# Optimization experiments

Measured on AMD Instinct MI355X. Metric: run time of the kernel, lower is better.

## Reference

```python
import jax, jax.numpy as jnp
import numpy as np

V, E, H = 32000, 256, 512
B, S, T = 32, 128, 64


def setup_inputs() -> dict:
    key = jax.random.key(0)
    ks = jax.random.split(key, 16)
    sc = 0.02
    n = lambda k, shp: (jax.random.normal(k, shp, jnp.float32) * sc)
    return {
        "src": jax.random.randint(ks[0], (B, S), 0, V),
        "tgt": jax.random.randint(ks[1], (B, T), 0, V),
        "embed": n(ks[2], (V, E)),
        "enc_Wih": n(ks[3], (4 * H, E)),
        "enc_Whh": n(ks[4], (4 * H, H)),
        "enc_bih": n(ks[5], (4 * H,)),
        "enc_bhh": n(ks[6], (4 * H,)),
        "dec_Wih": n(ks[7], (4 * H, E + H)),
        "dec_Whh": n(ks[8], (4 * H, H)),
        "dec_bih": n(ks[9], (4 * H,)),
        "dec_bhh": n(ks[10], (4 * H,)),
        "attn_W": n(ks[11], (H, 2 * H)),
        "attn_b": n(ks[12], (H,)),
        "attn_v": jax.random.uniform(ks[13], (H,), jnp.float32),  # torch.rand init
        "fc_W": n(ks[14], (V, H)),
        "fc_b": n(ks[15], (V,)),
    }


def lstm_step(x, h, c, Wih, Whh, bih, bhh):
    # PyTorch gate order: i, f, g, o
    gates = x @ Wih.T + h @ Whh.T + (bih + bhh)
    i, f, g, o = jnp.split(gates, 4, axis=-1)
    c = jax.nn.sigmoid(f) * c + jax.nn.sigmoid(i) * jnp.tanh(g)
    h = jax.nn.sigmoid(o) * jnp.tanh(c)
    return h, c


def reference(src, tgt, embed, enc_Wih, enc_Whh, enc_bih, enc_bhh,
              dec_Wih, dec_Whh, dec_bih, dec_bhh,
              attn_W, attn_b, attn_v, fc_W, fc_b):
    Bsz = src.shape[0]
    Hd = enc_Whh.shape[1]
    src_emb = embed[src]                      # [B,S,E]
    h0 = jnp.zeros((Bsz, Hd), jnp.float32)
    c0 = jnp.zeros((Bsz, Hd), jnp.float32)

    def enc_step(carry, x_t):
        h, c = carry
        h, c = lstm_step(x_t, h, c, enc_Wih, enc_Whh, enc_bih, enc_bhh)
        return (h, c), h

    (h, c), enc_hs = jax.lax.scan(enc_step, (h0, c0), src_emb.transpose(1, 0, 2))
    enc_out = enc_hs.transpose(1, 0, 2)       # [B,S,H]

    # split attn linear: W_attn @ cat(h, enc) = W_h @ h + W_e @ enc; precompute enc part
    W_h, W_e = attn_W[:, :Hd], attn_W[:, Hd:]
    enc_proj = jnp.einsum('bsh,kh->bsk', enc_out, W_e) + attn_b  # [B,S,H]

    dec_in = embed[tgt[:, :-1]]               # [B,T-1,E]

    def dec_step(carry, x_t):
        h, c = carry
        energy = jnp.tanh((h @ W_h.T)[:, None, :] + enc_proj)    # [B,S,H]
        scores = jnp.einsum('bsh,h->bs', energy, attn_v)
        w = jax.nn.softmax(scores, axis=1)
        context = jnp.einsum('bs,bsh->bh', w, enc_out)
        h, c = lstm_step(jnp.concatenate([x_t, context], axis=1), h, c,
                         dec_Wih, dec_Whh, dec_bih, dec_bhh)
        return (h, c), h

    (_, _), hs = jax.lax.scan(dec_step, (h, c), dec_in.transpose(1, 0, 2))
    outputs = jnp.einsum('tbh,vh->btv', hs, fc_W) + fc_b          # [B,T-1,V]
    return outputs
```

## Files before the change

### kernel.cpp

```cpp
#include <hip/hip_runtime.h>
#include <cstdint>
#include <cstddef>

typedef __bf16 bf16;
typedef __bf16 bf16x8 __attribute__((ext_vector_type(8)));
typedef __bf16 bf16x4 __attribute__((ext_vector_type(4)));
typedef float  f32x4  __attribute__((ext_vector_type(4)));

#define NV 32000
#define NE 256
#define NH 512
#define NB 32
#define NS 128
#define NT 64
#define NTD 63
#define G4H 2048

__device__ __forceinline__ float sigf(float x) {
    return 1.0f / (1.0f + __expf(-x));
}
__device__ __forceinline__ float tanhf_(float x) {
    return 1.0f - 2.0f / (__expf(2.0f * x) + 1.0f);
}

__global__ void k_cast_fcW(const float* __restrict__ src, bf16* __restrict__ dst, int n4) {
    int i = blockIdx.x * 256 + threadIdx.x;
    if (i < n4) {
        float4 v = *(const float4*)(src + 4 * (size_t)i);
        bf16x4 o;
        o[0] = (bf16)v.x; o[1] = (bf16)v.y; o[2] = (bf16)v.z; o[3] = (bf16)v.w;
        *(bf16x4*)(dst + 4 * (size_t)i) = o;
    }
}

__global__ void k_cast_small(const float* __restrict__ encWih, const float* __restrict__ decWih,
                             const float* __restrict__ attnW,
                             const float* __restrict__ ebih, const float* __restrict__ ebhh,
                             const float* __restrict__ dbih, const float* __restrict__ dbhh,
                             bf16* __restrict__ encWihB, bf16* __restrict__ decWihXB,
                             bf16* __restrict__ attnWeB,
                             float* __restrict__ bsumE, float* __restrict__ bsumD,
                             float* __restrict__ cbuf) {
    int i = blockIdx.x * 256 + threadIdx.x;
    const int n1 = G4H * NE;
    const int n2 = G4H * NE;
    const int n3 = NH * NH;
    if (i < n1) { encWihB[i] = (bf16)encWih[i]; return; }
    i -= n1;
    if (i < n2) { int r = i >> 8, c = i & 255; decWihXB[i] = (bf16)decWih[(size_t)r * 768 + c]; return; }
    i -= n2;
    if (i < n3) { int r = i >> 9, c = i & 511; attnWeB[i] = (bf16)attnW[(size_t)r * 1024 + 512 + c]; return; }
    i -= n3;
    if (i < G4H) { bsumE[i] = ebih[i] + ebhh[i]; return; }
    i -= G4H;
    if (i < G4H) { bsumD[i] = dbih[i] + dbhh[i]; return; }
    i -= G4H;
    if (i < NB * NH) { cbuf[i] = 0.0f; return; }
}

__global__ void k_embed(const int* __restrict__ src, const int* __restrict__ tgt,
                        const float* __restrict__ embed,
                        bf16* __restrict__ srcE, bf16* __restrict__ decE) {
    int i = blockIdx.x * 256 + threadIdx.x;
    const int nS = NB * NS * NE;
    if (i < nS) {
        int r = i >> 8, e = i & 255;
        srcE[i] = (bf16)embed[(size_t)src[r] * NE + e];
        return;
    }
    i -= nS;
    const int nD = NB * NTD * NE;
    if (i < nD) {
        int r = i >> 8, e = i & 255;
        int bb = r / NTD, tt = r % NTD;
        decE[i] = (bf16)embed[(size_t)tgt[bb * NT + tt] * NE + e];
    }
}

__global__ __launch_bounds__(256) void k_gemm(const bf16* __restrict__ A,
                                              const bf16* __restrict__ Bw,
                                              const float* __restrict__ bias,
                                              float* __restrict__ C,
                                              int M, int N, int K) {
    const int bn = blockIdx.x * 128;
    const int bm = blockIdx.y * 128;
    const int tid = threadIdx.x;
    __shared__ bf16 As[128 * 72];
    __shared__ bf16 Bs[128 * 72];
    const int wave = tid >> 6, lane = tid & 63;
    const int wm = (wave >> 1) * 64, wn = (wave & 1) * 64;
    const int r16 = lane & 15, quad = lane >> 4;

    f32x4 acc[4][4];
#pragma unroll
    for (int i = 0; i < 4; i++)
#pragma unroll
        for (int j = 0; j < 4; j++)
#pragma unroll
            for (int e = 0; e < 4; e++) acc[i][j][e] = 0.0f;

    for (int kb = 0; kb < K; kb += 64) {
#pragma unroll
        for (int i = 0; i < 4; i++) {
            int ci = tid + i * 256;
            int row = ci >> 3, kc = (ci & 7) * 8;
            bf16x8 va;
#pragma unroll
            for (int z = 0; z < 8; z++) va[z] = (bf16)0.0f;
            int gr = bm + row;
            if (gr < M) va = *(const bf16x8*)(A + (size_t)gr * K + kb + kc);
            *(bf16x8*)(As + row * 72 + kc) = va;
            bf16x8 vb = *(const bf16x8*)(Bw + (size_t)(bn + row) * K + kb + kc);
            *(bf16x8*)(Bs + row * 72 + kc) = vb;
        }
        __syncthreads();
#pragma unroll
        for (int ks = 0; ks < 2; ks++) {
            bf16x8 af[4], bfr[4];
#pragma unroll
            for (int mi = 0; mi < 4; mi++)
                af[mi] = *(const bf16x8*)(As + (wm + mi * 16 + r16) * 72 + ks * 32 + quad * 8);
#pragma unroll
            for (int ni = 0; ni < 4; ni++)
                bfr[ni] = *(const bf16x8*)(Bs + (wn + ni * 16 + r16) * 72 + ks * 32 + quad * 8);
#pragma unroll
            for (int mi = 0; mi < 4; mi++)
#pragma unroll
                for (int ni = 0; ni < 4; ni++)
                    acc[mi][ni] = __builtin_amdgcn_mfma_f32_16x16x32_bf16(af[mi], bfr[ni], acc[mi][ni], 0, 0, 0);
        }
        __syncthreads();
    }
#pragma unroll
    for (int mi = 0; mi < 4; mi++) {
#pragma unroll
        for (int e = 0; e < 4; e++) {
            int row = bm + wm + mi * 16 + quad * 4 + e;
            if (row < M) {
#pragma unroll
                for (int ni = 0; ni < 4; ni++) {
                    int col = bn + wn + ni * 16 + r16;
                    C[(size_t)row * N + col] = acc[mi][ni][e] + bias[col];
                }
            }
        }
    }
}

__global__ __launch_bounds__(256) void k_enc_step(const float* __restrict__ Xenc,
                                                  const float* __restrict__ Whh,
                                                  float* __restrict__ enc_out,
                                                  bf16* __restrict__ enc_out_b,
                                                  float* __restrict__ cbuf, int t) {
    const int blk = blockIdx.x;
    const int d0 = blk * 4;
    const int tid = threadIdx.x;
    __shared__ float wl[16 * 516];
    __shared__ float gl[16 * 33];

#pragma unroll
    for (int i = 0; i < 8; i++) {
        int ci = tid + i * 256;
        int ri = ci >> 7, kc = (ci & 127) * 4;
        int j = ((ri >> 2) * NH) + d0 + (ri & 3);
        *(float4*)(wl + ri * 516 + kc) = *(const float4*)(Whh + (size_t)j * NH + kc);
    }
    __syncthreads();

    const int b = tid >> 3, rl = tid & 7;
    float a0 = 0.0f, a1 = 0.0f;
    if (t > 0) {
        const float* hb = enc_out + ((size_t)(b * NS + t - 1)) * NH;
        const float* w0 = wl + rl * 516;
        const float* w1 = wl + (rl + 8) * 516;
        for (int kc = 0; kc < NH; kc += 4) {
            float4 h4 = *(const float4*)(hb + kc);
            float4 x0 = *(const float4*)(w0 + kc);
            float4 x1 = *(const float4*)(w1 + kc);
            a0 += h4.x * x0.x + h4.y * x0.y + h4.z * x0.z + h4.w * x0.w;
            a1 += h4.x * x1.x + h4.y * x1.y + h4.z * x1.z + h4.w * x1.w;
        }
    }
    {
        int j0 = ((rl >> 2) * NH) + d0 + (rl & 3);
        int j1 = (((rl + 8) >> 2) * NH) + d0 + ((rl + 8) & 3);
        const float* xr = Xenc + ((size_t)(b * NS + t)) * G4H;
        a0 += xr[j0];
        a1 += xr[j1];
        gl[rl * 33 + b] = a0;
        gl[(rl + 8) * 33 + b] = a1;
    }
    __syncthreads();
    if (tid < 128) {
        int bb = tid & 31, dl = tid >> 5;
        float gi = gl[(0 * 4 + dl) * 33 + bb];
        float gf = gl[(1 * 4 + dl) * 33 + bb];
        float gg = gl[(2 * 4 + dl) * 33 + bb];
        float go = gl[(3 * 4 + dl) * 33 + bb];
        int d = d0 + dl;
        float c_old = cbuf[bb * NH + d];
        float cn = sigf(gf) * c_old + sigf(gi) * tanhf_(gg);
        float hn = sigf(go) * tanhf_(cn);
        cbuf[bb * NH + d] = cn;
        size_t oi = ((size_t)(bb * NS + t)) * NH + d;
        enc_out[oi] = hn;
        enc_out_b[oi] = (bf16)hn;
    }
}

__global__ __launch_bounds__(256) void k_dec_mm1(const float* __restrict__ decWhh,
                                                 const float* __restrict__ attnW,
                                                 const float* __restrict__ enc_out,
                                                 const float* __restrict__ hbuf,
                                                 float* __restrict__ Gp,
                                                 float* __restrict__ hWh, int t) {
    const int blk = blockIdx.x;
    const int tid = threadIdx.x;
    __shared__ float wl[16 * 516];
    const bool gatePart = blk < 128;

#pragma unroll
    for (int i = 0; i < 8; i++) {
        int ci = tid + i * 256;
        int ri = ci >> 7, kc = (ci & 127) * 4;
        const float* srcp;
        if (gatePart) srcp = decWhh + (size_t)(blk * 16 + ri) * NH + kc;
        else          srcp = attnW + (size_t)((blk - 128) * 16 + ri) * 1024 + kc;
        *(float4*)(wl + ri * 516 + kc) = *(const float4*)srcp;
    }
    __syncthreads();

    const int b = tid >> 3, rl = tid & 7;
    const float* hb;
    if (t == 0) hb = enc_out + ((size_t)(b * NS + NS - 1)) * NH;
    else        hb = hbuf + (size_t)b * NH;
    const float* w0 = wl + rl * 516;
    const float* w1 = wl + (rl + 8) * 516;
    float a0 = 0.0f, a1 = 0.0f;
    for (int kc = 0; kc < NH; kc += 4) {
        float4 h4 = *(const float4*)(hb + kc);
        float4 x0 = *(const float4*)(w0 + kc);
        float4 x1 = *(const float4*)(w1 + kc);
        a0 += h4.x * x0.x + h4.y * x0.y + h4.z * x0.z + h4.w * x0.w;
        a1 += h4.x * x1.x + h4.y * x1.y + h4.z * x1.z + h4.w * x1.w;
    }
    if (gatePart) {
        int j0 = blk * 16 + rl;
        Gp[b * G4H + j0] = a0;
        Gp[b * G4H + j0 + 8] = a1;
    } else {
        int r0 = (blk - 128) * 16 + rl;
        hWh[b * NH + r0] = a0;
        hWh[b * NH + r0 + 8] = a1;
    }
}

__global__ __launch_bounds__(256) void k_dec_attn(const float* __restrict__ hWh,
                                                  const float* __restrict__ attn_v,
                                                  const float* __restrict__ enc_proj,
                                                  const float* __restrict__ enc_out,
                                                  float* __restrict__ ctx) {
    const int b = blockIdx.x;
    const int tid = threadIdx.x;
    __shared__ float hw[512], vv[512], ps[256], sc[128], red[64];
    hw[tid] = hWh[b * NH + tid];
    hw[tid + 256] = hWh[b * NH + tid + 256];
    vv[tid] = attn_v[tid];
    vv[tid + 256] = attn_v[tid + 256];
    __syncthreads();

    const int s = tid >> 1, hf = tid & 1;
    const float* ep = enc_proj + ((size_t)(b * NS + s)) * NH + hf * 256;
    const float* hwp = hw + hf * 256;
    const float* vvp = vv + hf * 256;
    float p = 0.0f;
    for (int k = 0; k < 256; k += 4) {
        float4 e = *(const float4*)(ep + k);
        p += tanhf_(hwp[k + 0] + e.x) * vvp[k + 0];
        p += tanhf_(hwp[k + 1] + e.y) * vvp[k + 1];
        p += tanhf_(hwp[k + 2] + e.z) * vvp[k + 2];
        p += tanhf_(hwp[k + 3] + e.w) * vvp[k + 3];
    }
    ps[tid] = p;
    __syncthreads();
    if (tid < 128) sc[tid] = ps[2 * tid] + ps[2 * tid + 1];
    __syncthreads();
    if (tid < 64) red[tid] = fmaxf(sc[tid], sc[tid + 64]);
    __syncthreads();
    if (tid < 32) red[tid] = fmaxf(red[tid], red[tid + 32]);
    __syncthreads();
    if (tid < 16) red[tid] = fmaxf(red[tid], red[tid + 16]);
    __syncthreads();
    if (tid < 8) red[tid] = fmaxf(red[tid], red[tid + 8]);
    __syncthreads();
    if (tid < 4) red[tid] = fmaxf(red[tid], red[tid + 4]);
    __syncthreads();
    if (tid < 2) red[tid] = fmaxf(red[tid], red[tid + 2]);
    __syncthreads();
    if (tid == 0) red[0] = fmaxf(red[0], red[1]);
    __syncthreads();
    float mx = red[0];
    __syncthreads();
    if (tid < 128) sc[tid] = __expf(sc[tid] - mx);
    __syncthreads();
    if (tid < 64) red[tid] = sc[tid] + sc[tid + 64];
    __syncthreads();
    if (tid < 32) red[tid] = red[tid] + red[tid + 32];
    __syncthreads();
    if (tid < 16) red[tid] = red[tid] + red[tid + 16];
    __syncthreads();
    if (tid < 8) red[tid] = red[tid] + red[tid + 8];
    __syncthreads();
    if (tid < 4) red[tid] = red[tid] + red[tid + 4];
    __syncthreads();
    if (tid < 2) red[tid] = red[tid] + red[tid + 2];
    __syncthreads();
    if (tid == 0) red[0] = red[0] + red[1];
    __syncthreads();
    float inv = 1.0f / red[0];
    __syncthreads();
    if (tid < 128) sc[tid] *= inv;
    __syncthreads();
#pragma unroll
    for (int half = 0; half < 2; half++) {
        int k = tid + half * 256;
        float a = 0.0f;
        const float* eo = enc_out + ((size_t)(b * NS)) * NH + k;
        for (int s2 = 0; s2 < NS; s2++) a += sc[s2] * eo[(size_t)s2 * NH];
        ctx[b * NH + k] = a;
    }
}

__global__ __launch_bounds__(256) void k_dec_final(const float* __restrict__ Xdec,
                                                   const float* __restrict__ decWih,
                                                   const float* __restrict__ Gp,
                                                   const float* __restrict__ ctx,
                                                   float* __restrict__ cbuf,
                                                   float* __restrict__ hbuf,
                                                   bf16* __restrict__ hs_b, int t) {
    const int blk = blockIdx.x;
    const int d0 = blk * 4;
    const int tid = threadIdx.x;
    __shared__ float wl[16 * 516];
    __shared__ float gl[16 * 33];

#pragma unroll
    for (int i = 0; i < 8; i++) {
        int ci = tid + i * 256;
        int ri = ci >> 7, kc = (ci & 127) * 4;
        int j = ((ri >> 2) * NH) + d0 + (ri & 3);
        *(float4*)(wl + ri * 516 + kc) = *(const float4*)(decWih + (size_t)j * 768 + 256 + kc);
    }
    __syncthreads();

    const int b = tid >> 3, rl = tid & 7;
    const float* cb = ctx + (size_t)b * NH;
    const float* w0 = wl + rl * 516;
    const float* w1 = wl + (rl + 8) * 516;
    float a0 = 0.0f, a1 = 0.0f;
    for (int kc = 0; kc < NH; kc += 4) {
        float4 h4 = *(const float4*)(cb + kc);
        float4 x0 = *(const float4*)(w0 + kc);
        float4 x1 = *(const float4*)(w1 + kc);
        a0 += h4.x * x0.x + h4.y * x0.y + h4.z * x0.z + h4.w * x0.w;
        a1 += h4.x * x1.x + h4.y * x1.y + h4.z * x1.z + h4.w * x1.w;
    }
    {
        int j0 = ((rl >> 2) * NH) + d0 + (rl & 3);
        int j1 = (((rl + 8) >> 2) * NH) + d0 + ((rl + 8) & 3);
        const float* xr = Xdec + ((size_t)(b * NTD + t)) * G4H;
        a0 += xr[j0] + Gp[b * G4H + j0];
        a1 += xr[j1] + Gp[b * G4H + j1];
        gl[rl * 33 + b] = a0;
        gl[(rl + 8) * 33 + b] = a1;
    }
    __syncthreads();
    if (tid < 128) {
        int bb = tid & 31, dl = tid >> 5;
        float gi = gl[(0 * 4 + dl) * 33 + bb];
        float gf = gl[(1 * 4 + dl) * 33 + bb];
        float gg = gl[(2 * 4 + dl) * 33 + bb];
        float go = gl[(3 * 4 + dl) * 33 + bb];
        int d = d0 + dl;
        float c_old = cbuf[bb * NH + d];
        float cn = sigf(gf) * c_old + sigf(gi) * tanhf_(gg);
        float hn = sigf(go) * tanhf_(cn);
        cbuf[bb * NH + d] = cn;
        hbuf[bb * NH + d] = hn;
        hs_b[((size_t)(bb * NTD + t)) * NH + d] = (bf16)hn;
    }
}

extern "C" void kernel_launch(void* const* d_in, const int* in_sizes, int n_in,
                              void* d_out, int out_size, void* d_ws, size_t ws_size,
                              hipStream_t stream) {
    const int* src = (const int*)d_in[0];
    const int* tgt = (const int*)d_in[1];
    const float* embed = (const float*)d_in[2];
    const float* encWih = (const float*)d_in[3];
    const float* encWhh = (const float*)d_in[4];
    const float* encbih = (const float*)d_in[5];
    const float* encbhh = (const float*)d_in[6];
    const float* decWih = (const float*)d_in[7];
    const float* decWhh = (const float*)d_in[8];
    const float* decbih = (const float*)d_in[9];
    const float* decbhh = (const float*)d_in[10];
    const float* attnW = (const float*)d_in[11];
    const float* attnb = (const float*)d_in[12];
    const float* attnv = (const float*)d_in[13];
    const float* fcW = (const float*)d_in[14];
    const float* fcb = (const float*)d_in[15];
    float* out = (float*)d_out;

    char* w = (char*)d_ws;
    auto alloc = [&](size_t bytes) -> char* {
        char* p = w;
        w += (bytes + 255) & ~(size_t)255;
        return p;
    };
    bf16* fcWB     = (bf16*)alloc((size_t)NV * NH * 2);
    bf16* encWihB  = (bf16*)alloc((size_t)G4H * NE * 2);
    bf16* decWihXB = (bf16*)alloc((size_t)G4H * NE * 2);
    bf16* attnWeB  = (bf16*)alloc((size_t)NH * NH * 2);
    bf16* srcE     = (bf16*)alloc((size_t)NB * NS * NE * 2);
    bf16* decE     = (bf16*)alloc((size_t)NB * NTD * NE * 2);
    float* bsumE   = (float*)alloc((size_t)G4H * 4);
    float* bsumD   = (float*)alloc((size_t)G4H * 4);
    float* Xenc    = (float*)alloc((size_t)NB * NS * G4H * 4);
    float* Xdec    = (float*)alloc((size_t)NB * NTD * G4H * 4);
    float* enc_out = (float*)alloc((size_t)NB * NS * NH * 4);
    bf16* enc_outB = (bf16*)alloc((size_t)NB * NS * NH * 2);
    float* encproj = (float*)alloc((size_t)NB * NS * NH * 4);
    float* cbuf    = (float*)alloc((size_t)NB * NH * 4);
    float* hbuf    = (float*)alloc((size_t)NB * NH * 4);
    float* Gp      = (float*)alloc((size_t)NB * G4H * 4);
    float* hWh     = (float*)alloc((size_t)NB * NH * 4);
    float* ctx     = (float*)alloc((size_t)NB * NH * 4);
    bf16* hsB      = (bf16*)alloc((size_t)NB * NTD * NH * 2);
    (void)ws_size; (void)in_sizes; (void)n_in; (void)out_size;

    {
        int n4 = NV * NH / 4;
        k_cast_fcW<<<(n4 + 255) / 256, 256, 0, stream>>>(fcW, fcWB, n4);
        int tot = G4H * NE + G4H * NE + NH * NH + G4H + G4H + NB * NH;
        k_cast_small<<<(tot + 255) / 256, 256, 0, stream>>>(encWih, decWih, attnW,
                                                            encbih, encbhh, decbih, decbhh,
                                                            encWihB, decWihXB, attnWeB,
                                                            bsumE, bsumD, cbuf);
        int te = NB * NS * NE + NB * NTD * NE;
        k_embed<<<(te + 255) / 256, 256, 0, stream>>>(src, tgt, embed, srcE, decE);
    }
    k_gemm<<<dim3(G4H / 128, (NB * NS) / 128), 256, 0, stream>>>(srcE, encWihB, bsumE, Xenc,
                                                                 NB * NS, G4H, NE);
    k_gemm<<<dim3(G4H / 128, (NB * NTD + 127) / 128), 256, 0, stream>>>(decE, decWihXB, bsumD, Xdec,
                                                                        NB * NTD, G4H, NE);
    for (int t = 0; t < NS; t++)
        k_enc_step<<<128, 256, 0, stream>>>(Xenc, encWhh, enc_out, enc_outB, cbuf, t);
    k_gemm<<<dim3(NH / 128, (NB * NS) / 128), 256, 0, stream>>>(enc_outB, attnWeB, attnb, encproj,
                                                                NB * NS, NH, NH);
    for (int t = 0; t < NTD; t++) {
        k_dec_mm1<<<160, 256, 0, stream>>>(decWhh, attnW, enc_out, hbuf, Gp, hWh, t);
        k_dec_attn<<<32, 256, 0, stream>>>(hWh, attnv, encproj, enc_out, ctx);
        k_dec_final<<<128, 256, 0, stream>>>(Xdec, decWih, Gp, ctx, cbuf, hbuf, hsB, t);
    }
    k_gemm<<<dim3(NV / 128, (NB * NTD + 127) / 128), 256, 0, stream>>>(hsB, fcWB, fcb, out,
                                                                       NB * NTD, NV, NH);
}
```

Before: 4.636 ms.

## Make encoder and decoder loops persistent kernels with a software grid barrier

Replaces the 128 per-timestep encoder launches and the 63×3 decoder launches with one persistent kernel each. A global atomic grid barrier separates the time steps, and the cell state stays in registers. Weights are no longer staged in shared memory each step; they are read straight from global memory (cache-resident) through a dot product with split accumulators. This removes launch overhead and repeated weight staging, but relies on all 128/160 blocks being co-resident for the spin barrier, which risks deadlock if they are not.

New measurement: 14.38 ms. +210.1%, slower.

```diff
diff --git a/kernel.cpp b/kernel.cpp
--- a/kernel.cpp
+++ b/kernel.cpp
@@ -23,6 +23,45 @@
     return 1.0f - 2.0f / (__expf(2.0f * x) + 1.0f);
 }
 
+__device__ __forceinline__ void gridbar(unsigned* bar, unsigned nb) {
+    __syncthreads();
+    if (threadIdx.x == 0) {
+        unsigned g = __hip_atomic_load(bar + 16, __ATOMIC_RELAXED, __HIP_MEMORY_SCOPE_AGENT);
+        unsigned prev = __hip_atomic_fetch_add(bar, 1u, __ATOMIC_ACQ_REL, __HIP_MEMORY_SCOPE_AGENT);
+        if (prev == nb - 1u) {
+            __hip_atomic_store(bar, 0u, __ATOMIC_RELAXED, __HIP_MEMORY_SCOPE_AGENT);
+            __hip_atomic_store(bar + 16, g + 1u, __ATOMIC_RELEASE, __HIP_MEMORY_SCOPE_AGENT);
+        } else {
+            while (__hip_atomic_load(bar + 16, __ATOMIC_RELAXED, __HIP_MEMORY_SCOPE_AGENT) == g)
+                __builtin_amdgcn_s_sleep(2);
+            __threadfence();
+        }
+    }
+    __syncthreads();
+}
+
+__device__ __forceinline__ void dot2_512(const float* __restrict__ hb,
+                                         const float* __restrict__ w0,
+                                         const float* __restrict__ w1,
+                                         float& a0, float& a1) {
+    float s00 = 0.f, s01 = 0.f, s10 = 0.f, s11 = 0.f;
+#pragma unroll 4
+    for (int kc = 0; kc < NH; kc += 8) {
+        float4 hA = *(const float4*)(hb + kc);
+        float4 hB = *(const float4*)(hb + kc + 4);
+        float4 x0A = *(const float4*)(w0 + kc);
+        float4 x0B = *(const float4*)(w0 + kc + 4);
+        float4 x1A = *(const float4*)(w1 + kc);
+        float4 x1B = *(const float4*)(w1 + kc + 4);
+        s00 += hA.x * x0A.x + hA.y * x0A.y + hA.z * x0A.z + hA.w * x0A.w;
+        s01 += hB.x * x0B.x + hB.y * x0B.y + hB.z * x0B.z + hB.w * x0B.w;
+        s10 += hA.x * x1A.x + hA.y * x1A.y + hA.z * x1A.z + hA.w * x1A.w;
+        s11 += hB.x * x1B.x + hB.y * x1B.y + hB.z * x1B.z + hB.w * x1B.w;
+    }
+    a0 += s00 + s01;
+    a1 += s10 + s11;
+}
+
 __global__ void k_cast_fcW(const float* __restrict__ src, bf16* __restrict__ dst, int n4) {
     int i = blockIdx.x * 256 + threadIdx.x;
     if (i < n4) {
@@ -40,7 +79,7 @@
                              bf16* __restrict__ encWihB, bf16* __restrict__ decWihXB,
                              bf16* __restrict__ attnWeB,
                              float* __restrict__ bsumE, float* __restrict__ bsumD,
-                             float* __restrict__ cbuf) {
+                             float* __restrict__ cbuf, unsigned* __restrict__ bar) {
     int i = blockIdx.x * 256 + threadIdx.x;
     const int n1 = G4H * NE;
     const int n2 = G4H * NE;
@@ -56,6 +95,8 @@
     if (i < G4H) { bsumD[i] = dbih[i] + dbhh[i]; return; }
     i -= G4H;
     if (i < NB * NH) { cbuf[i] = 0.0f; return; }
+    i -= NB * NH;
+    if (i < 32) { bar[i] = 0u; return; }
 }
 
 __global__ void k_embed(const int* __restrict__ src, const int* __restrict__ tgt,
@@ -147,247 +188,212 @@
     }
 }
 
-__global__ __launch_bounds__(256) void k_enc_step(const float* __restrict__ Xenc,
-                                                  const float* __restrict__ Whh,
-                                                  float* __restrict__ enc_out,
-                                                  bf16* __restrict__ enc_out_b,
-                                                  float* __restrict__ cbuf, int t) {
+__global__ __launch_bounds__(256) void k_enc_all(const float* __restrict__ Xenc,
+                                                 const float* __restrict__ Whh,
+                                                 float* __restrict__ enc_out,
+                                                 bf16* __restrict__ enc_out_b,
+                                                 float* __restrict__ cbuf,
+                                                 unsigned* __restrict__ bar) {
     const int blk = blockIdx.x;
     const int d0 = blk * 4;
     const int tid = threadIdx.x;
-    __shared__ float wl[16 * 516];
     __shared__ float gl[16 * 33];
 
-#pragma unroll
-    for (int i = 0; i < 8; i++) {
-        int ci = tid + i * 256;
-        int ri = ci >> 7, kc = (ci & 127) * 4;
-        int j = ((ri >> 2) * NH) + d0 + (ri & 3);
-        *(float4*)(wl + ri * 516 + kc) = *(const float4*)(Whh + (size_t)j * NH + kc);
-    }
-    __syncthreads();
-
     const int b = tid >> 3, rl = tid & 7;
-    float a0 = 0.0f, a1 = 0.0f;
-    if (t > 0) {
-        const float* hb = enc_out + ((size_t)(b * NS + t - 1)) * NH;
-        const float* w0 = wl + rl * 516;
-        const float* w1 = wl + (rl + 8) * 516;
-        for (int kc = 0; kc < NH; kc += 4) {
-            float4 h4 = *(const float4*)(hb + kc);
-            float4 x0 = *(const float4*)(w0 + kc);
-            float4 x1 = *(const float4*)(w1 + kc);
-            a0 += h4.x * x0.x + h4.y * x0.y + h4.z * x0.z + h4.w * x0.w;
-            a1 += h4.x * x1.x + h4.y * x1.y + h4.z * x1.z + h4.w * x1.w;
-        }
-    }
-    {
-        int j0 = ((rl >> 2) * NH) + d0 + (rl & 3);
-        int j1 = (((rl + 8) >> 2) * NH) + d0 + ((rl + 8) & 3);
+    const int j0 = ((rl >> 2) * NH) + d0 + (rl & 3);
+    const int j1 = (((rl + 8) >> 2) * NH) + d0 + ((rl + 8) & 3);
+    const float* w0 = Whh + (size_t)j0 * NH;
+    const float* w1 = Whh + (size_t)j1 * NH;
+
+    const int bb = tid & 31, dl = (tid >> 5) & 3;
+    const int d = d0 + dl;
+    float creg = 0.0f;
+
+    const unsigned nb = gridDim.x;
+    for (int t = 0; t < NS; t++) {
         const float* xr = Xenc + ((size_t)(b * NS + t)) * G4H;
-        a0 += xr[j0];
-        a1 += xr[j1];
+        float a0 = xr[j0], a1 = xr[j1];
+        if (t > 0) {
+            const float* hb = enc_out + ((size_t)(b * NS + t - 1)) * NH;
+            dot2_512(hb, w0, w1, a0, a1);
+        }
         gl[rl * 33 + b] = a0;
         gl[(rl + 8) * 33 + b] = a1;
-    }
-    __syncthreads();
-    if (tid < 128) {
-        int bb = tid & 31, dl = tid >> 5;
-        float gi = gl[(0 * 4 + dl) * 33 + bb];
-        float gf = gl[(1 * 4 + dl) * 33 + bb];
-        float gg = gl[(2 * 4 + dl) * 33 + bb];
-        float go = gl[(3 * 4 + dl) * 33 + bb];
-        int d = d0 + dl;
-        float c_old = cbuf[bb * NH + d];
-        float cn = sigf(gf) * c_old + sigf(gi) * tanhf_(gg);
-        float hn = sigf(go) * tanhf_(cn);
-        cbuf[bb * NH + d] = cn;
-        size_t oi = ((size_t)(bb * NS + t)) * NH + d;
-        enc_out[oi] = hn;
-        enc_out_b[oi] = (bf16)hn;
-    }
-}
-
-__global__ __launch_bounds__(256) void k_dec_mm1(const float* __restrict__ decWhh,
+        __syncthreads();
+        if (tid < 128) {
+            float gi = gl[(0 * 4 + dl) * 33 + bb];
+            float gf = gl[(1 * 4 + dl) * 33 + bb];
+            float gg = gl[(2 * 4 + dl) * 33 + bb];
+            float go = gl[(3 * 4 + dl) * 33 + bb];
+            float cn = sigf(gf) * creg + sigf(gi) * tanhf_(gg);
+            float hn = sigf(go) * tanhf_(cn);
+            creg = cn;
+            size_t oi = ((size_t)(bb * NS + t)) * NH + d;
+            enc_out[oi] = hn;
+            enc_out_b[oi] = (bf16)hn;
+        }
+        gridbar(bar, nb);
+    }
+    if (tid < 128) cbuf[bb * NH + d] = creg;
+}
+
+__global__ __launch_bounds__(256) void k_dec_all(const float* __restrict__ decWhh,
                                                  const float* __restrict__ attnW,
+                                                 const float* __restrict__ attn_v,
                                                  const float* __restrict__ enc_out,
-                                                 const float* __restrict__ hbuf,
+                                                 const float* __restrict__ enc_proj,
+                                                 const float* __restrict__ Xdec,
+                                                 const float* __restrict__ decWih,
                                                  float* __restrict__ Gp,
-                                                 float* __restrict__ hWh, int t) {
+                                                 float* __restrict__ hWh,
+                                                 float* __restrict__ ctx,
+                                                 const float* __restrict__ cbuf,
+                                                 float* __restrict__ hbuf,
+                                                 bf16* __restrict__ hs_b,
+                                                 unsigned* __restrict__ bar) {
     const int blk = blockIdx.x;
     const int tid = threadIdx.x;
-    __shared__ float wl[16 * 516];
+    __shared__ float gl[16 * 33];
+    __shared__ float hw[512], vv[512], ps[256], scb[128], red[64];
+
+    const int b8 = tid >> 3, rl = tid & 7;
     const bool gatePart = blk < 128;
 
-#pragma unroll
-    for (int i = 0; i < 8; i++) {
-        int ci = tid + i * 256;
-        int ri = ci >> 7, kc = (ci & 127) * 4;
-        const float* srcp;
-        if (gatePart) srcp = decWhh + (size_t)(blk * 16 + ri) * NH + kc;
-        else          srcp = attnW + (size_t)((blk - 128) * 16 + ri) * 1024 + kc;
-        *(float4*)(wl + ri * 516 + kc) = *(const float4*)srcp;
-    }
-    __syncthreads();
-
-    const int b = tid >> 3, rl = tid & 7;
-    const float* hb;
-    if (t == 0) hb = enc_out + ((size_t)(b * NS + NS - 1)) * NH;
-    else        hb = hbuf + (size_t)b * NH;
-    const float* w0 = wl + rl * 516;
-    const float* w1 = wl + (rl + 8) * 516;
-    float a0 = 0.0f, a1 = 0.0f;
-    for (int kc = 0; kc < NH; kc += 4) {
-        float4 h4 = *(const float4*)(hb + kc);
-        float4 x0 = *(const float4*)(w0 + kc);
-        float4 x1 = *(const float4*)(w1 + kc);
-        a0 += h4.x * x0.x + h4.y * x0.y + h4.z * x0.z + h4.w * x0.w;
-        a1 += h4.x * x1.x + h4.y * x1.y + h4.z * x1.z + h4.w * x1.w;
-    }
+    const float *w0p1, *w1p1;
+    int p1j0;
     if (gatePart) {
-        int j0 = blk * 16 + rl;
-        Gp[b * G4H + j0] = a0;
-        Gp[b * G4H + j0 + 8] = a1;
+        int j = blk * 16 + rl;
+        w0p1 = decWhh + (size_t)j * NH;
+        w1p1 = decWhh + (size_t)(j + 8) * NH;
+        p1j0 = j;
     } else {
-        int r0 = (blk - 128) * 16 + rl;
-        hWh[b * NH + r0] = a0;
-        hWh[b * NH + r0 + 8] = a1;
-    }
-}
-
-__global__ __launch_bounds__(256) void k_dec_attn(const float* __restrict__ hWh,
-                                                  const float* __restrict__ attn_v,
-                                                  const float* __restrict__ enc_proj,
-                                                  const float* __restrict__ enc_out,
-                                                  float* __restrict__ ctx) {
-    const int b = blockIdx.x;
-    const int tid = threadIdx.x;
-    __shared__ float hw[512], vv[512], ps[256], sc[128], red[64];
-    hw[tid] = hWh[b * NH + tid];
-    hw[tid + 256] = hWh[b * NH + tid + 256];
-    vv[tid] = attn_v[tid];
-    vv[tid + 256] = attn_v[tid + 256];
-    __syncthreads();
-
-    const int s = tid >> 1, hf = tid & 1;
-    const float* ep = enc_proj + ((size_t)(b * NS + s)) * NH + hf * 256;
-    const float* hwp = hw + hf * 256;
-    const float* vvp = vv + hf * 256;
-    float p = 0.0f;
-    for (int k = 0; k < 256; k += 4) {
-        float4 e = *(const float4*)(ep + k);
-        p += tanhf_(hwp[k + 0] + e.x) * vvp[k + 0];
-        p += tanhf_(hwp[k + 1] + e.y) * vvp[k + 1];
-        p += tanhf_(hwp[k + 2] + e.z) * vvp[k + 2];
-        p += tanhf_(hwp[k + 3] + e.w) * vvp[k + 3];
-    }
-    ps[tid] = p;
-    __syncthreads();
-    if (tid < 128) sc[tid] = ps[2 * tid] + ps[2 * tid + 1];
-    __syncthreads();
-    if (tid < 64) red[tid] = fmaxf(sc[tid], sc[tid + 64]);
-    __syncthreads();
-    if (tid < 32) red[tid] = fmaxf(red[tid], red[tid + 32]);
-    __syncthreads();
-    if (tid < 16) red[tid] = fmaxf(red[tid], red[tid + 16]);
-    __syncthreads();
-    if (tid < 8) red[tid] = fmaxf(red[tid], red[tid + 8]);
-    __syncthreads();
-    if (tid < 4) red[tid] = fmaxf(red[tid], red[tid + 4]);
-    __syncthreads();
-    if (tid < 2) red[tid] = fmaxf(red[tid], red[tid + 2]);
-    __syncthreads();
-    if (tid == 0) red[0] = fmaxf(red[0], red[1]);
-    __syncthreads();
-    float mx = red[0];
-    __syncthreads();
-    if (tid < 128) sc[tid] = __expf(sc[tid] - mx);
-    __syncthreads();
-    if (tid < 64) red[tid] = sc[tid] + sc[tid + 64];
-    __syncthreads();
-    if (tid < 32) red[tid] = red[tid] + red[tid + 32];
-    __syncthreads();
-    if (tid < 16) red[tid] = red[tid] + red[tid + 16];
-    __syncthreads();
-    if (tid < 8) red[tid] = red[tid] + red[tid + 8];
-    __syncthreads();
-    if (tid < 4) red[tid] = red[tid] + red[tid + 4];
-    __syncthreads();
-    if (tid < 2) red[tid] = red[tid] + red[tid + 2];
-    __syncthreads();
-    if (tid == 0) red[0] = red[0] + red[1];
-    __syncthreads();
-    float inv = 1.0f / red[0];
-    __syncthreads();
-    if (tid < 128) sc[tid] *= inv;
-    __syncthreads();
-#pragma unroll
-    for (int half = 0; half < 2; half++) {
-        int k = tid + half * 256;
-        float a = 0.0f;
-        const float* eo = enc_out + ((size_t)(b * NS)) * NH + k;
-        for (int s2 = 0; s2 < NS; s2++) a += sc[s2] * eo[(size_t)s2 * NH];
-        ctx[b * NH + k] = a;
-    }
-}
-
-__global__ __launch_bounds__(256) void k_dec_final(const float* __restrict__ Xdec,
-                                                   const float* __restrict__ decWih,
-                                                   const float* __restrict__ Gp,
-                                                   const float* __restrict__ ctx,
-                                                   float* __restrict__ cbuf,
-                                                   float* __restrict__ hbuf,
-                                                   bf16* __restrict__ hs_b, int t) {
-    const int blk = blockIdx.x;
+        int r = (blk - 128) * 16 + rl;
+        w0p1 = attnW + (size_t)r * 1024;
+        w1p1 = attnW + (size_t)(r + 8) * 1024;
+        p1j0 = r;
+    }
+
     const int d0 = blk * 4;
-    const int tid = threadIdx.x;
-    __shared__ float wl[16 * 516];
-    __shared__ float gl[16 * 33];
-
-#pragma unroll
-    for (int i = 0; i < 8; i++) {
-        int ci = tid + i * 256;
-        int ri = ci >> 7, kc = (ci & 127) * 4;
-        int j = ((ri >> 2) * NH) + d0 + (ri & 3);
-        *(float4*)(wl + ri * 516 + kc) = *(const float4*)(decWih + (size_t)j * 768 + 256 + kc);
-    }
-    __syncthreads();
-
-    const int b = tid >> 3, rl = tid & 7;
-    const float* cb = ctx + (size_t)b * NH;
-    const float* w0 = wl + rl * 516;
-    const float* w1 = wl + (rl + 8) * 516;
-    float a0 = 0.0f, a1 = 0.0f;
-    for (int kc = 0; kc < NH; kc += 4) {
-        float4 h4 = *(const float4*)(cb + kc);
-        float4 x0 = *(const float4*)(w0 + kc);
-        float4 x1 = *(const float4*)(w1 + kc);
-        a0 += h4.x * x0.x + h4.y * x0.y + h4.z * x0.z + h4.w * x0.w;
-        a1 += h4.x * x1.x + h4.y * x1.y + h4.z * x1.z + h4.w * x1.w;
-    }
-    {
-        int j0 = ((rl >> 2) * NH) + d0 + (rl & 3);
-        int j1 = (((rl + 8) >> 2) * NH) + d0 + ((rl + 8) & 3);
-        const float* xr = Xdec + ((size_t)(b * NTD + t)) * G4H;
-        a0 += xr[j0] + Gp[b * G4H + j0];
-        a1 += xr[j1] + Gp[b * G4H + j1];
-        gl[rl * 33 + b] = a0;
-        gl[(rl + 8) * 33 + b] = a1;
-    }
-    __syncthreads();
-    if (tid < 128) {
-        int bb = tid & 31, dl = tid >> 5;
-        float gi = gl[(0 * 4 + dl) * 33 + bb];
-        float gf = gl[(1 * 4 + dl) * 33 + bb];
-        float gg = gl[(2 * 4 + dl) * 33 + bb];
-        float go = gl[(3 * 4 + dl) * 33 + bb];
-        int d = d0 + dl;
-        float c_old = cbuf[bb * NH + d];
-        float cn = sigf(gf) * c_old + sigf(gi) * tanhf_(gg);
-        float hn = sigf(go) * tanhf_(cn);
-        cbuf[bb * NH + d] = cn;
-        hbuf[bb * NH + d] = hn;
-        hs_b[((size_t)(bb * NTD + t)) * NH + d] = (bf16)hn;
+    const int j0 = ((rl >> 2) * NH) + d0 + (rl & 3);
+    const int j1 = (((rl + 8) >> 2) * NH) + d0 + ((rl + 8) & 3);
+    const float* w0p3 = decWih + (size_t)j0 * 768 + 256;
+    const float* w1p3 = decWih + (size_t)j1 * 768 + 256;
+
+    const int bb = tid & 31, dl = (tid >> 5) & 3;
+    const int d = d0 + dl;
+    float creg = (gatePart && tid < 128) ? cbuf[bb * NH + d] : 0.0f;
+
+    const unsigned nb = gridDim.x;
+    for (int t = 0; t < NTD; t++) {
+        {
+            const float* hb = (t == 0) ? enc_out + ((size_t)(b8 * NS + NS - 1)) * NH
+                                       : hbuf + (size_t)b8 * NH;
+            float a0 = 0.0f, a1 = 0.0f;
+            dot2_512(hb, w0p1, w1p1, a0, a1);
+            if (gatePart) {
+                Gp[b8 * G4H + p1j0] = a0;
+                Gp[b8 * G4H + p1j0 + 8] = a1;
+            } else {
+                hWh[b8 * NH + p1j0] = a0;
+                hWh[b8 * NH + p1j0 + 8] = a1;
+            }
+        }
+        gridbar(bar, nb);
+
+        if (blk < 32) {
+            const int b = blk;
+            hw[tid] = hWh[b * NH + tid];
+            hw[tid + 256] = hWh[b * NH + tid + 256];
+            vv[tid] = attn_v[tid];
+            vv[tid + 256] = attn_v[tid + 256];
+            __syncthreads();
+
+            const int s = tid >> 1, hf = tid & 1;
+            const float* ep = enc_proj + ((size_t)(b * NS + s)) * NH + hf * 256;
+            const float* hwp = hw + hf * 256;
+            const float* vvp = vv + hf * 256;
+            float p = 0.0f;
+            for (int k = 0; k < 256; k += 4) {
+                float4 e = *(const float4*)(ep + k);
+                p += tanhf_(hwp[k + 0] + e.x) * vvp[k + 0];
+                p += tanhf_(hwp[k + 1] + e.y) * vvp[k + 1];
+                p += tanhf_(hwp[k + 2] + e.z) * vvp[k + 2];
+                p += tanhf_(hwp[k + 3] + e.w) * vvp[k + 3];
+            }
+            ps[tid] = p;
+            __syncthreads();
+            if (tid < 128) scb[tid] = ps[2 * tid] + ps[2 * tid + 1];
+            __syncthreads();
+            if (tid < 64) red[tid] = fmaxf(scb[tid], scb[tid + 64]);
+            __syncthreads();
+            if (tid < 32) red[tid] = fmaxf(red[tid], red[tid + 32]);
+            __syncthreads();
+            if (tid < 16) red[tid] = fmaxf(red[tid], red[tid + 16]);
+            __syncthreads();
+            if (tid < 8) red[tid] = fmaxf(red[tid], red[tid + 8]);
+            __syncthreads();
+            if (tid < 4) red[tid] = fmaxf(red[tid], red[tid + 4]);
+            __syncthreads();
+            if (tid < 2) red[tid] = fmaxf(red[tid], red[tid + 2]);
+            __syncthreads();
+            if (tid == 0) red[0] = fmaxf(red[0], red[1]);
+            __syncthreads();
+            float mx = red[0];
+            __syncthreads();
+            if (tid < 128) scb[tid] = __expf(scb[tid] - mx);
+            __syncthreads();
+            if (tid < 64) red[tid] = scb[tid] + scb[tid + 64];
+            __syncthreads();
+            if (tid < 32) red[tid] = red[tid] + red[tid + 32];
+            __syncthreads();
+            if (tid < 16) red[tid] = red[tid] + red[tid + 16];
+            __syncthreads();
+            if (tid < 8) red[tid] = red[tid] + red[tid + 8];
+            __syncthreads();
+            if (tid < 4) red[tid] = red[tid] + red[tid + 4];
+            __syncthreads();
+            if (tid < 2) red[tid] = red[tid] + red[tid + 2];
+            __syncthreads();
+            if (tid == 0) red[0] = red[0] + red[1];
+            __syncthreads();
+            float inv = 1.0f / red[0];
+            __syncthreads();
+            if (tid < 128) scb[tid] *= inv;
+            __syncthreads();
+#pragma unroll
+            for (int half = 0; half < 2; half++) {
+                int k = tid + half * 256;
+                float a = 0.0f;
+                const float* eo = enc_out + ((size_t)(b * NS)) * NH + k;
+                for (int s2 = 0; s2 < NS; s2++) a += scb[s2] * eo[(size_t)s2 * NH];
+                ctx[b * NH + k] = a;
+            }
+        }
+        gridbar(bar, nb);
+
+        if (gatePart) {
+            const float* cb = ctx + (size_t)b8 * NH;
+            float a0 = 0.0f, a1 = 0.0f;
+            dot2_512(cb, w0p3, w1p3, a0, a1);
+            const float* xr = Xdec + ((size_t)(b8 * NTD + t)) * G4H;
+            a0 += xr[j0] + Gp[b8 * G4H + j0];
+            a1 += xr[j1] + Gp[b8 * G4H + j1];
+            gl[rl * 33 + b8] = a0;
+            gl[(rl + 8) * 33 + b8] = a1;
+            __syncthreads();
+            if (tid < 128) {
+                float gi = gl[(0 * 4 + dl) * 33 + bb];
+                float gf = gl[(1 * 4 + dl) * 33 + bb];
+                float gg = gl[(2 * 4 + dl) * 33 + bb];
+                float go = gl[(3 * 4 + dl) * 33 + bb];
+                float cn = sigf(gf) * creg + sigf(gi) * tanhf_(gg);
+                float hn = sigf(go) * tanhf_(cn);
+                creg = cn;
+                hbuf[bb * NH + d] = hn;
+                hs_b[((size_t)(bb * NTD + t)) * NH + d] = (bf16)hn;
+            }
+        }
+        gridbar(bar, nb);
     }
 }
 
@@ -437,16 +443,17 @@
     float* hWh     = (float*)alloc((size_t)NB * NH * 4);
     float* ctx     = (float*)alloc((size_t)NB * NH * 4);
     bf16* hsB      = (bf16*)alloc((size_t)NB * NTD * NH * 2);
+    unsigned* bar  = (unsigned*)alloc(256);
     (void)ws_size; (void)in_sizes; (void)n_in; (void)out_size;
 
     {
         int n4 = NV * NH / 4;
         k_cast_fcW<<<(n4 + 255) / 256, 256, 0, stream>>>(fcW, fcWB, n4);
-        int tot = G4H * NE + G4H * NE + NH * NH + G4H + G4H + NB * NH;
+        int tot = G4H * NE + G4H * NE + NH * NH + G4H + G4H + NB * NH + 32;
         k_cast_small<<<(tot + 255) / 256, 256, 0, stream>>>(encWih, decWih, attnW,
                                                             encbih, encbhh, decbih, decbhh,
                                                             encWihB, decWihXB, attnWeB,
-                                                            bsumE, bsumD, cbuf);
+                                                            bsumE, bsumD, cbuf, bar);
         int te = NB * NS * NE + NB * NTD * NE;
         k_embed<<<(te + 255) / 256, 256, 0, stream>>>(src, tgt, embed, srcE, decE);
     }
@@ -454,15 +461,11 @@
                                                                  NB * NS, G4H, NE);
     k_gemm<<<dim3(G4H / 128, (NB * NTD + 127) / 128), 256, 0, stream>>>(decE, decWihXB, bsumD, Xdec,
                                                                         NB * NTD, G4H, NE);
-    for (int t = 0; t < NS; t++)
-        k_enc_step<<<128, 256, 0, stream>>>(Xenc, encWhh, enc_out, enc_outB, cbuf, t);
+    k_enc_all<<<128, 256, 0, stream>>>(Xenc, encWhh, enc_out, enc_outB, cbuf, bar);
     k_gemm<<<dim3(NH / 128, (NB * NS) / 128), 256, 0, stream>>>(enc_outB, attnWeB, attnb, encproj,
                                                                 NB * NS, NH, NH);
-    for (int t = 0; t < NTD; t++) {
-        k_dec_mm1<<<160, 256, 0, stream>>>(decWhh, attnW, enc_out, hbuf, Gp, hWh, t);
-        k_dec_attn<<<32, 256, 0, stream>>>(hWh, attnv, encproj, enc_out, ctx);
-        k_dec_final<<<128, 256, 0, stream>>>(Xdec, decWih, Gp, ctx, cbuf, hbuf, hsB, t);
-    }
+    k_dec_all<<<160, 256, 0, stream>>>(decWhh, attnW, attnv, enc_out, encproj, Xdec, decWih,
+                                       Gp, hWh, ctx, cbuf, hbuf, hsB, bar);
     k_gemm<<<dim3(NV / 128, (NB * NTD + 127) / 128), 256, 0, stream>>>(hsB, fcWB, fcb, out,
                                                                        NB * NTD, NV, NH);
 }
```
